# Kernel tuning notes

Hardware: AMD Instinct MI355X
Metric: run time of the kernel (lower is better)

The kernel has to match this reference:

```python
import jax, jax.numpy as jnp
import numpy as np
import math

# ---- static circuit structure ----
N_QUBITS = 12
N_STATES = 1 << N_QUBITS
NUM_HEADS = 4
HEAD_DIM = N_QUBITS // NUM_HEADS
EPS = 1e-5

# convention: wire 0 = most significant bit of the basis index
_idx = np.arange(N_STATES)
_bits = (_idx[:, None] >> (N_QUBITS - 1 - np.arange(N_QUBITS))) & 1  # (N_STATES, n)
SIGNS = jnp.asarray((1 - 2 * _bits).astype(np.float32))  # +1 for |0>, -1 for |1>

# compose the CNOT ring [(0,1),(1,2),...,(n-2,n-1),(n-1,0)] into a single basis permutation.
# each CNOT(c,t) maps basis b -> b xor (bit_c(b) << pos_t); applying gate G: new[b] = old[sigma(b)].
_perm = _idx.copy()
_gates = [(i, i + 1) for i in range(N_QUBITS - 1)] + [(N_QUBITS - 1, 0)]
for _c, _t in reversed(_gates):
    _bc = (_idx >> (N_QUBITS - 1 - _c)) & 1
    _sigma = _idx ^ (_bc << (N_QUBITS - 1 - _t))
    _perm = _sigma[_perm]
PERM = jnp.asarray(_perm.astype(np.int32))
# second rx layer uses params token[wire % head_dim]
FOLD = np.arange(N_QUBITS) % HEAD_DIM


def _ring_z(theta):
    """Per-token circuit: RX(theta_k) on wire k (the two consecutive RX layers are
    pre-summed into theta), then CNOT ring, then <Z_k> for every wire.
    Product-state probabilities suffice: CNOTs only permute the computational basis.
    theta: (..., n_qubits) -> (..., n_qubits) expectation values."""
    shp = theta.shape
    T = theta.reshape(-1, N_QUBITS)
    h = 0.5 * T
    p0 = jnp.cos(h) ** 2  # P(|0>) per qubit after RX(theta)|0>
    p1 = jnp.sin(h) ** 2
    probs = jnp.ones((T.shape[0], 1), T.dtype)
    for k in range(N_QUBITS):  # kron build, wire 0 is MSB -> (tokens, 2^n)
        pk = jnp.stack([p0[:, k], p1[:, k]], axis=-1)
        probs = (probs[:, :, None] * pk[:, None, :]).reshape(T.shape[0], -1)
    probs = probs[:, PERM]  # apply CNOT ring as basis permutation
    return (probs @ SIGNS).reshape(shp)


def _layernorm(x, g, b):
    mu = jnp.mean(x, axis=-1, keepdims=True)
    var = jnp.mean((x - mu) ** 2, axis=-1, keepdims=True)
    return (x - mu) * jax.lax.rsqrt(var + EPS) * g + b


def _forward(x, wq, wk, wv, wo, w1, b1, w2, b2, g1, be1, g2, be2):
    B, S, E = x.shape
    # multi-head attention (dropout in eval mode = identity)
    q = (x @ wq).reshape(B, S, NUM_HEADS, HEAD_DIM).transpose(0, 2, 1, 3)
    k = (x @ wk).reshape(B, S, NUM_HEADS, HEAD_DIM).transpose(0, 2, 1, 3)
    v = (x @ wv).reshape(B, S, NUM_HEADS, HEAD_DIM).transpose(0, 2, 1, 3)
    scores = jnp.einsum('bhqd,bhkd->bhqk', q, k) / math.sqrt(HEAD_DIM)
    attn = jax.nn.softmax(scores, axis=-1)
    o = jnp.einsum('bhqk,bhkd->bhqd', attn, v).transpose(0, 2, 1, 3).reshape(B, S, E)
    # per-token quantum circuit: encoder RX(o_k) then RX(o_{k % head_dim}) combine additively
    theta = o + o[..., FOLD]
    attn_out = _ring_z(theta) @ wo
    x1 = _layernorm(x + attn_out, g1, be1)
    # quantum FFN: RX(h_k) then RY(h_k) on |0>, no entangler -> <Z_k> = cos(h_k)*cos(h_k)
    hdn = jax.nn.relu(x1 @ w1 + b1)
    zq = jnp.cos(hdn) * jnp.cos(hdn)
    ffn_out = zq @ w2 + b2
    return _layernorm(x1 + ffn_out, g2, be2)


def setup_inputs() -> dict:
    key = jax.random.key(0)
    ks = jax.random.split(key, 8)
    E = N_QUBITS
    F = N_QUBITS  # ffn_dim forced equal to n_qubits by the source
    s = 1.0 / math.sqrt(E)
    return {
        'x': jax.random.normal(ks[0], (4, 2048, E), jnp.float32),
        'wq': jax.random.normal(ks[1], (E, E), jnp.float32) * s,
        'wk': jax.random.normal(ks[2], (E, E), jnp.float32) * s,
        'wv': jax.random.normal(ks[3], (E, E), jnp.float32) * s,
        'wo': jax.random.normal(ks[4], (E, E), jnp.float32) * s,
        'w1': jax.random.normal(ks[5], (E, F), jnp.float32) * s,
        'b1': jnp.zeros((F,), jnp.float32),
        'w2': jax.random.normal(ks[6], (F, E), jnp.float32) * (1.0 / math.sqrt(F)),
        'b2': jnp.zeros((E,), jnp.float32),
        'g1': jnp.ones((E,), jnp.float32),
        'be1': jnp.zeros((E,), jnp.float32),
        'g2': jnp.ones((E,), jnp.float32),
        'be2': jnp.zeros((E,), jnp.float32),
    }


def reference(x, wq, wk, wv, wo, w1, b1, w2, b2, g1, be1, g2, be2):
    return _forward(x, wq, wk, wv, wo, w1, b1, w2, b2, g1, be1, g2, be2)
```

## Files before the change

kernel.cpp:

```cpp
#include <hip/hip_runtime.h>
#include <math.h>

#define S_LEN 2048
#define NB 4
#define NH 4
#define BHN 16
#define E_DIM 12
#define NKB 8
#define KEYS_PER_KB (S_LEN / NKB)
#define NQT 8
#define QT_SIZE (S_LEN / NQT)
#define QSCALE 0.8329931278350429f

__global__ __launch_bounds__(256) void attn_kernel(
    const float* __restrict__ x,
    const float* __restrict__ wq, const float* __restrict__ wk,
    const float* __restrict__ wv, float4* __restrict__ part)
{
    __shared__ float4 sK[KEYS_PER_KB];
    __shared__ float4 sV[KEYS_PER_KB];
    __shared__ float4 sQ[QT_SIZE];
    __shared__ float  sw[108];
    __shared__ float4 sAcc[4 * QT_SIZE];

    int tid = threadIdx.x;
    int kb = blockIdx.x & (NKB - 1);
    int qt = (blockIdx.x / NKB) & (NQT - 1);
    int bh = blockIdx.x / (NKB * NQT);
    int b  = bh >> 2;
    int h  = bh & 3;

    if (tid < 108) {
        int m = tid / 36;
        int i = tid - m * 36;
        int e = i / 3, d = i - e * 3;
        const float* w = (m == 0) ? wq : (m == 1) ? wk : wv;
        sw[tid] = w[e * 12 + h * 3 + d];
    }
    __syncthreads();

    {
        size_t kt = (size_t)b * S_LEN + kb * KEYS_PER_KB + tid;
        const float4* xp = (const float4*)(x + kt * E_DIM);
        float4 xa = xp[0], xb = xp[1], xc = xp[2];
        float xr[12] = {xa.x, xa.y, xa.z, xa.w, xb.x, xb.y, xb.z, xb.w, xc.x, xc.y, xc.z, xc.w};
        float k0 = 0, k1 = 0, k2 = 0, v0 = 0, v1 = 0, v2 = 0;
#pragma unroll
        for (int e = 0; e < 12; ++e) {
            float xe = xr[e];
            k0 = fmaf(xe, sw[36 + e * 3 + 0], k0);
            k1 = fmaf(xe, sw[36 + e * 3 + 1], k1);
            k2 = fmaf(xe, sw[36 + e * 3 + 2], k2);
            v0 = fmaf(xe, sw[72 + e * 3 + 0], v0);
            v1 = fmaf(xe, sw[72 + e * 3 + 1], v1);
            v2 = fmaf(xe, sw[72 + e * 3 + 2], v2);
        }
        sK[tid] = make_float4(k0, k1, k2, 0.0f);
        sV[tid] = make_float4(v0, v1, v2, 1.0f);

        size_t qtk = (size_t)b * S_LEN + qt * QT_SIZE + tid;
        const float4* xq = (const float4*)(x + qtk * E_DIM);
        float4 qa = xq[0], qb = xq[1], qc = xq[2];
        float qr[12] = {qa.x, qa.y, qa.z, qa.w, qb.x, qb.y, qb.z, qb.w, qc.x, qc.y, qc.z, qc.w};
        float q0 = 0, q1 = 0, q2 = 0;
#pragma unroll
        for (int e = 0; e < 12; ++e) {
            float xe = qr[e];
            q0 = fmaf(xe, sw[e * 3 + 0], q0);
            q1 = fmaf(xe, sw[e * 3 + 1], q1);
            q2 = fmaf(xe, sw[e * 3 + 2], q2);
        }
        sQ[tid] = make_float4(q0 * QSCALE, q1 * QSCALE, q2 * QSCALE, 0.0f);
    }
    __syncthreads();

    int w = tid >> 6;
    int lane = tid & 63;

    float4 q[4];
#pragma unroll
    for (int r = 0; r < 4; ++r) q[r] = sQ[r * 64 + lane];

    float4 acc[4];
#pragma unroll
    for (int r = 0; r < 4; ++r) acc[r] = make_float4(0.f, 0.f, 0.f, 0.f);

    int kbeg = w * 64;
#pragma unroll 4
    for (int j = 0; j < 64; ++j) {
        float4 kk = sK[kbeg + j];
        float4 vv = sV[kbeg + j];
#pragma unroll
        for (int r = 0; r < 4; ++r) {
            float sc = fmaf(q[r].x, kk.x, fmaf(q[r].y, kk.y, q[r].z * kk.z));
            float p = __builtin_amdgcn_exp2f(sc);
            acc[r].x = fmaf(p, vv.x, acc[r].x);
            acc[r].y = fmaf(p, vv.y, acc[r].y);
            acc[r].z = fmaf(p, vv.z, acc[r].z);
            acc[r].w = fmaf(p, vv.w, acc[r].w);
        }
    }

#pragma unroll
    for (int r = 0; r < 4; ++r) sAcc[w * QT_SIZE + r * 64 + lane] = acc[r];
    __syncthreads();

    float4 sum = sAcc[tid];
    float4 p1 = sAcc[QT_SIZE + tid];
    float4 p2 = sAcc[2 * QT_SIZE + tid];
    float4 p3 = sAcc[3 * QT_SIZE + tid];
    sum.x += p1.x + p2.x + p3.x;
    sum.y += p1.y + p2.y + p3.y;
    sum.z += p1.z + p2.z + p3.z;
    sum.w += p1.w + p2.w + p3.w;

    part[((size_t)kb * BHN + bh) * S_LEN + qt * QT_SIZE + tid] = sum;
}

__global__ __launch_bounds__(128) void tail_kernel(
    const float4* __restrict__ part, const float* __restrict__ x,
    const float* __restrict__ wo, const float* __restrict__ w1, const float* __restrict__ b1,
    const float* __restrict__ w2, const float* __restrict__ b2,
    const float* __restrict__ g1, const float* __restrict__ be1,
    const float* __restrict__ g2, const float* __restrict__ be2,
    float* __restrict__ out)
{
    __shared__ float swo[144], sw1[144], sw2[144];
    __shared__ float sb1[12], sb2[12], sg1[12], sbe1[12], sg2[12], sbe2[12];
    int tid = threadIdx.x;
    for (int i = tid; i < 144; i += 128) { swo[i] = wo[i]; sw1[i] = w1[i]; sw2[i] = w2[i]; }
    if (tid < 12) {
        sb1[tid] = b1[tid]; sb2[tid] = b2[tid];
        sg1[tid] = g1[tid]; sbe1[tid] = be1[tid];
        sg2[tid] = g2[tid]; sbe2[tid] = be2[tid];
    }
    __syncthreads();

    int t = blockIdx.x * 128 + tid;
    int b = t >> 11;
    int s = t & (S_LEN - 1);

    float o[12];
#pragma unroll
    for (int h = 0; h < NH; ++h) {
        int bh = b * NH + h;
        float ax = 0, ay = 0, az = 0, aw = 0;
#pragma unroll
        for (int kb = 0; kb < NKB; ++kb) {
            float4 p = part[((size_t)kb * BHN + bh) * S_LEN + s];
            ax += p.x; ay += p.y; az += p.z; aw += p.w;
        }
        float inv = 1.0f / aw;
        o[h * 3 + 0] = ax * inv;
        o[h * 3 + 1] = ay * inv;
        o[h * 3 + 2] = az * inv;
    }

    float c[12];
#pragma unroll
    for (int k = 0; k < 12; ++k) c[k] = __cosf(o[k] + o[k % 3]);

    float z[12];
    {
        float p = c[0];
#pragma unroll
        for (int k = 1; k < 12; ++k) { p *= c[k]; z[k] = p; }
        p = c[1];
#pragma unroll
        for (int k = 2; k < 12; ++k) p *= c[k];
        z[0] = p;
    }

    const float4* xp = (const float4*)(x + (size_t)t * E_DIM);
    float4 xa = xp[0], xb = xp[1], xc = xp[2];
    float xr[12] = {xa.x, xa.y, xa.z, xa.w, xb.x, xb.y, xb.z, xb.w, xc.x, xc.y, xc.z, xc.w};

    float y[12];
#pragma unroll
    for (int e = 0; e < 12; ++e) {
        float ao = 0;
#pragma unroll
        for (int k = 0; k < 12; ++k) ao = fmaf(z[k], swo[k * 12 + e], ao);
        y[e] = xr[e] + ao;
    }

    float mu = 0;
#pragma unroll
    for (int e = 0; e < 12; ++e) mu += y[e];
    mu *= (1.0f / 12.0f);
    float var = 0;
#pragma unroll
    for (int e = 0; e < 12; ++e) { float d = y[e] - mu; var = fmaf(d, d, var); }
    var *= (1.0f / 12.0f);
    float rs = rsqrtf(var + 1e-5f);
    float x1v[12];
#pragma unroll
    for (int e = 0; e < 12; ++e) x1v[e] = (y[e] - mu) * rs * sg1[e] + sbe1[e];

    float zq[12];
#pragma unroll
    for (int f = 0; f < 12; ++f) {
        float hd = sb1[f];
#pragma unroll
        for (int e = 0; e < 12; ++e) hd = fmaf(x1v[e], sw1[e * 12 + f], hd);
        hd = fmaxf(hd, 0.0f);
        float cc = __cosf(hd);
        zq[f] = cc * cc;
    }
    float y2[12];
#pragma unroll
    for (int e = 0; e < 12; ++e) {
        float fo = sb2[e];
#pragma unroll
        for (int f = 0; f < 12; ++f) fo = fmaf(zq[f], sw2[f * 12 + e], fo);
        y2[e] = x1v[e] + fo;
    }

    float mu2 = 0;
#pragma unroll
    for (int e = 0; e < 12; ++e) mu2 += y2[e];
    mu2 *= (1.0f / 12.0f);
    float var2 = 0;
#pragma unroll
    for (int e = 0; e < 12; ++e) { float d = y2[e] - mu2; var2 = fmaf(d, d, var2); }
    var2 *= (1.0f / 12.0f);
    float rs2 = rsqrtf(var2 + 1e-5f);

    float res[12];
#pragma unroll
    for (int e = 0; e < 12; ++e) res[e] = (y2[e] - mu2) * rs2 * sg2[e] + sbe2[e];

    float4* op = (float4*)(out + (size_t)t * E_DIM);
    op[0] = make_float4(res[0], res[1], res[2], res[3]);
    op[1] = make_float4(res[4], res[5], res[6], res[7]);
    op[2] = make_float4(res[8], res[9], res[10], res[11]);
}

extern "C" void kernel_launch(void* const* d_in, const int* in_sizes, int n_in,
                              void* d_out, int out_size, void* d_ws, size_t ws_size,
                              hipStream_t stream)
{
    const float* x   = (const float*)d_in[0];
    const float* wq  = (const float*)d_in[1];
    const float* wk  = (const float*)d_in[2];
    const float* wv  = (const float*)d_in[3];
    const float* wo  = (const float*)d_in[4];
    const float* w1  = (const float*)d_in[5];
    const float* b1  = (const float*)d_in[6];
    const float* w2  = (const float*)d_in[7];
    const float* b2  = (const float*)d_in[8];
    const float* g1  = (const float*)d_in[9];
    const float* be1 = (const float*)d_in[10];
    const float* g2  = (const float*)d_in[11];
    const float* be2 = (const float*)d_in[12];

    float4* part = (float4*)d_ws;

    attn_kernel<<<BHN * NQT * NKB, 256, 0, stream>>>(x, wq, wk, wv, part);
    tail_kernel<<<64, 128, 0, stream>>>(part, x, wo, w1, b1, w2, b2,
                                        g1, be1, g2, be2, (float*)d_out);
}
```

Baseline: 27.89 us.

## Use packed FP32 math in attention loop, alias LDS, and retile tail

The attention inner loop now processes two queries at a time with v_pk_mul/v_pk_fma/v_pk_add inline asm, halving the VALU issue count for score and accumulation math. The denominator is kept as a separate packed add instead of multiplying by a constant 1 in V. Shared memory is unified into one 16 KB buffer where the accumulator reduction aliases K/V/Q, guarded by an extra barrier. Launch bounds request 6 blocks per CU to raise occupancy. The tail kernel is relaunched as 128 blocks of 64 threads to spread across more CUs. Risks are inline asm blocking scheduler optimizations and the added barrier.

```diff
diff --git a/kernel.cpp b/kernel.cpp
--- a/kernel.cpp
+++ b/kernel.cpp
@@ -2,7 +2,6 @@
 #include <math.h>
 
 #define S_LEN 2048
-#define NB 4
 #define NH 4
 #define BHN 16
 #define E_DIM 12
@@ -12,16 +11,36 @@
 #define QT_SIZE (S_LEN / NQT)
 #define QSCALE 0.8329931278350429f
 
-__global__ __launch_bounds__(256) void attn_kernel(
+typedef float f32x2 __attribute__((ext_vector_type(2)));
+
+static __device__ __forceinline__ f32x2 pk_mul_blo(f32x2 a, f32x2 b) {
+    f32x2 d; asm("v_pk_mul_f32 %0, %1, %2 op_sel_hi:[1,0]"
+                 : "=v"(d) : "v"(a), "v"(b)); return d;
+}
+static __device__ __forceinline__ f32x2 pk_fma_blo(f32x2 a, f32x2 b, f32x2 c) {
+    f32x2 d; asm("v_pk_fma_f32 %0, %1, %2, %3 op_sel_hi:[1,0,1]"
+                 : "=v"(d) : "v"(a), "v"(b), "v"(c)); return d;
+}
+static __device__ __forceinline__ f32x2 pk_fma_bhi(f32x2 a, f32x2 b, f32x2 c) {
+    f32x2 d; asm("v_pk_fma_f32 %0, %1, %2, %3 op_sel:[0,1,0] op_sel_hi:[1,1,1]"
+                 : "=v"(d) : "v"(a), "v"(b), "v"(c)); return d;
+}
+static __device__ __forceinline__ f32x2 pk_add2(f32x2 a, f32x2 b) {
+    f32x2 d; asm("v_pk_add_f32 %0, %1, %2"
+                 : "=v"(d) : "v"(a), "v"(b)); return d;
+}
+
+__global__ __launch_bounds__(256, 6) void attn_kernel(
     const float* __restrict__ x,
     const float* __restrict__ wq, const float* __restrict__ wk,
     const float* __restrict__ wv, float4* __restrict__ part)
 {
-    __shared__ float4 sK[KEYS_PER_KB];
-    __shared__ float4 sV[KEYS_PER_KB];
-    __shared__ float4 sQ[QT_SIZE];
-    __shared__ float  sw[108];
-    __shared__ float4 sAcc[4 * QT_SIZE];
+    __shared__ __align__(16) char smem[16384];
+    float4* sK  = (float4*)smem;
+    float4* sV  = sK + KEYS_PER_KB;
+    float4* sQ  = sV + KEYS_PER_KB;
+    float*  sw  = (float*)(smem + 12288);
+    float4* sAcc = (float4*)smem;
 
     int tid = threadIdx.x;
     int kb = blockIdx.x & (NKB - 1);
@@ -56,7 +75,7 @@
             v2 = fmaf(xe, sw[72 + e * 3 + 2], v2);
         }
         sK[tid] = make_float4(k0, k1, k2, 0.0f);
-        sV[tid] = make_float4(v0, v1, v2, 1.0f);
+        sV[tid] = make_float4(v0, v1, v2, 0.0f);
 
         size_t qtk = (size_t)b * S_LEN + qt * QT_SIZE + tid;
         const float4* xq = (const float4*)(x + qtk * E_DIM);
@@ -77,32 +96,51 @@
     int w = tid >> 6;
     int lane = tid & 63;
 
-    float4 q[4];
-#pragma unroll
-    for (int r = 0; r < 4; ++r) q[r] = sQ[r * 64 + lane];
-
-    float4 acc[4];
-#pragma unroll
-    for (int r = 0; r < 4; ++r) acc[r] = make_float4(0.f, 0.f, 0.f, 0.f);
+    float4 q0 = sQ[0 * 64 + lane];
+    float4 q1 = sQ[1 * 64 + lane];
+    float4 q2 = sQ[2 * 64 + lane];
+    float4 q3 = sQ[3 * 64 + lane];
+    f32x2 qx01 = {q0.x, q1.x}, qy01 = {q0.y, q1.y}, qz01 = {q0.z, q1.z};
+    f32x2 qx23 = {q2.x, q3.x}, qy23 = {q2.y, q3.y}, qz23 = {q2.z, q3.z};
+
+    f32x2 ax01 = {0,0}, ay01 = {0,0}, az01 = {0,0}, ad01 = {0,0};
+    f32x2 ax23 = {0,0}, ay23 = {0,0}, az23 = {0,0}, ad23 = {0,0};
 
     int kbeg = w * 64;
 #pragma unroll 4
     for (int j = 0; j < 64; ++j) {
         float4 kk = sK[kbeg + j];
         float4 vv = sV[kbeg + j];
-#pragma unroll
-        for (int r = 0; r < 4; ++r) {
-            float sc = fmaf(q[r].x, kk.x, fmaf(q[r].y, kk.y, q[r].z * kk.z));
-            float p = __builtin_amdgcn_exp2f(sc);
-            acc[r].x = fmaf(p, vv.x, acc[r].x);
-            acc[r].y = fmaf(p, vv.y, acc[r].y);
-            acc[r].z = fmaf(p, vv.z, acc[r].z);
-            acc[r].w = fmaf(p, vv.w, acc[r].w);
-        }
-    }
-
-#pragma unroll
-    for (int r = 0; r < 4; ++r) sAcc[w * QT_SIZE + r * 64 + lane] = acc[r];
+        f32x2 kxy = {kk.x, kk.y};
+        f32x2 kzw = {kk.z, kk.w};
+        f32x2 vxy = {vv.x, vv.y};
+        f32x2 vzw = {vv.z, vv.w};
+        f32x2 s01 = pk_mul_blo(qz01, kzw);
+        s01 = pk_fma_bhi(qy01, kxy, s01);
+        s01 = pk_fma_blo(qx01, kxy, s01);
+        f32x2 s23 = pk_mul_blo(qz23, kzw);
+        s23 = pk_fma_bhi(qy23, kxy, s23);
+        s23 = pk_fma_blo(qx23, kxy, s23);
+        f32x2 p01, p23;
+        p01.x = __builtin_amdgcn_exp2f(s01.x);
+        p01.y = __builtin_amdgcn_exp2f(s01.y);
+        p23.x = __builtin_amdgcn_exp2f(s23.x);
+        p23.y = __builtin_amdgcn_exp2f(s23.y);
+        ax01 = pk_fma_blo(p01, vxy, ax01);
+        ay01 = pk_fma_bhi(p01, vxy, ay01);
+        az01 = pk_fma_blo(p01, vzw, az01);
+        ad01 = pk_add2(p01, ad01);
+        ax23 = pk_fma_blo(p23, vxy, ax23);
+        ay23 = pk_fma_bhi(p23, vxy, ay23);
+        az23 = pk_fma_blo(p23, vzw, az23);
+        ad23 = pk_add2(p23, ad23);
+    }
+
+    __syncthreads();
+    sAcc[w * QT_SIZE + 0 * 64 + lane] = make_float4(ax01.x, ay01.x, az01.x, ad01.x);
+    sAcc[w * QT_SIZE + 1 * 64 + lane] = make_float4(ax01.y, ay01.y, az01.y, ad01.y);
+    sAcc[w * QT_SIZE + 2 * 64 + lane] = make_float4(ax23.x, ay23.x, az23.x, ad23.x);
+    sAcc[w * QT_SIZE + 3 * 64 + lane] = make_float4(ax23.y, ay23.y, az23.y, ad23.y);
     __syncthreads();
 
     float4 sum = sAcc[tid];
@@ -117,7 +155,7 @@
     part[((size_t)kb * BHN + bh) * S_LEN + qt * QT_SIZE + tid] = sum;
 }
 
-__global__ __launch_bounds__(128) void tail_kernel(
+__global__ __launch_bounds__(64) void tail_kernel(
     const float4* __restrict__ part, const float* __restrict__ x,
     const float* __restrict__ wo, const float* __restrict__ w1, const float* __restrict__ b1,
     const float* __restrict__ w2, const float* __restrict__ b2,
@@ -128,7 +166,7 @@
     __shared__ float swo[144], sw1[144], sw2[144];
     __shared__ float sb1[12], sb2[12], sg1[12], sbe1[12], sg2[12], sbe2[12];
     int tid = threadIdx.x;
-    for (int i = tid; i < 144; i += 128) { swo[i] = wo[i]; sw1[i] = w1[i]; sw2[i] = w2[i]; }
+    for (int i = tid; i < 144; i += 64) { swo[i] = wo[i]; sw1[i] = w1[i]; sw2[i] = w2[i]; }
     if (tid < 12) {
         sb1[tid] = b1[tid]; sb2[tid] = b2[tid];
         sg1[tid] = g1[tid]; sbe1[tid] = be1[tid];
@@ -136,7 +174,7 @@
     }
     __syncthreads();
 
-    int t = blockIdx.x * 128 + tid;
+    int t = blockIdx.x * 64 + tid;
     int b = t >> 11;
     int s = t & (S_LEN - 1);
 
@@ -257,6 +295,6 @@
     float4* part = (float4*)d_ws;
 
     attn_kernel<<<BHN * NQT * NKB, 256, 0, stream>>>(x, wq, wk, wv, part);
-    tail_kernel<<<64, 128, 0, stream>>>(part, x, wo, w1, b1, w2, b2,
+    tail_kernel<<<128, 64, 0, stream>>>(part, x, wo, w1, b1, w2, b2,
                                         g1, be1, g2, be2, (float*)d_out);
 }
```

Measured after the change: 25.91 us. 1.08x faster.
